# Performance work log

Hardware: AMD Instinct MI355X
Metric: run time of the kernel (lower is better)

## Reference

```python
import jax, jax.numpy as jnp
import numpy as np

N = 100000   # nodes
E = 1250000  # edges
F_IN = 64    # node feature dim
H = 64       # hidden_channels
B = 256      # graphs in batch
C = 2        # num_classes


def setup_inputs() -> dict:
    key = jax.random.key(0)
    ks = jax.random.split(key, 12)
    x = jax.random.normal(ks[0], (N, F_IN), dtype=jnp.float32)
    edge_index = jax.random.randint(ks[1], (2, E), 0, N, dtype=jnp.int64)
    batch = jnp.sort(jax.random.randint(ks[2], (N,), 0, B, dtype=jnp.int64))
    s = 1.0 / np.sqrt(H)
    W1 = jax.random.uniform(ks[3], (F_IN, H), jnp.float32, -s, s)
    b1 = jnp.zeros((H,), jnp.float32)
    W2 = jax.random.uniform(ks[4], (H, H), jnp.float32, -s, s)
    b2 = jnp.zeros((H,), jnp.float32)
    W3 = jax.random.uniform(ks[5], (H, H), jnp.float32, -s, s)
    b3 = jnp.zeros((H,), jnp.float32)
    Wl = jax.random.uniform(ks[6], (H, C), jnp.float32, -s, s)
    bl = jnp.zeros((C,), jnp.float32)
    return {"x": x, "edge_index": edge_index, "batch": batch,
            "W1": W1, "b1": b1, "W2": W2, "b2": b2, "W3": W3, "b3": b3,
            "Wl": Wl, "bl": bl}


def gcn_conv(x, W, b, src, dst, dinv_sqrt):
    # PyG GCNConv: h = x @ W; symmetric normalization with self-loops;
    # self-loop contribution handled analytically (norm = 1/deg).
    h = x @ W                                   # [N, H]
    norm = dinv_sqrt[src] * dinv_sqrt[dst]      # [E]
    msg = norm[:, None] * h[src]                # [E, H]
    agg = jax.ops.segment_sum(msg, dst, num_segments=x.shape[0])
    agg = agg + (dinv_sqrt * dinv_sqrt)[:, None] * h  # self loops
    return agg + b


def reference(x, edge_index, batch, W1, b1, W2, b2, W3, b3, Wl, bl):
    src, dst = edge_index[0], edge_index[1]
    # degree with self-loops (computed on target nodes, as in PyG)
    ones = jnp.ones((E,), jnp.float32)
    deg = jax.ops.segment_sum(ones, dst, num_segments=N) + 1.0
    dinv_sqrt = jax.lax.rsqrt(deg)

    h = jax.nn.relu(gcn_conv(x, W1, b1, src, dst, dinv_sqrt))
    h = jax.nn.relu(gcn_conv(h, W2, b2, src, dst, dinv_sqrt))
    h = gcn_conv(h, W3, b3, src, dst, dinv_sqrt)

    # global_mean_pool over batch vector
    sums = jax.ops.segment_sum(h, batch, num_segments=B)          # [B, H]
    cnts = jax.ops.segment_sum(jnp.ones((N,), jnp.float32), batch, num_segments=B)
    pooled = sums / jnp.maximum(cnts, 1.0)[:, None]

    # dropout(p=0.5) is identity in inference mode
    return pooled @ Wl + bl  # [B, C]
```

## Files before the change

kernel.cpp:

```cpp
#include <hip/hip_runtime.h>

#define NN 100000
#define EE 1250000
#define HH 64
#define BB 256
#define CC 2
#define NBLK 391
#define GBLK 2048
#define NWAVE (GBLK * 4)

__device__ __forceinline__ float lanebcast(float v, int k) {
    return __int_as_float(__builtin_amdgcn_readlane(__float_as_int(v), k));
}

__global__ void detect_i64(const int* __restrict__ raw, int* __restrict__ flag) {
    __shared__ int nonzero;
    if (threadIdx.x == 0) nonzero = 0;
    __syncthreads();
    int any = 0;
#pragma unroll
    for (int i = 0; i < 4; ++i) {
        int idx = 2 * (threadIdx.x + i * 256) + 1;
        if (raw[idx] != 0) any = 1;
    }
    if (any) atomicOr(&nonzero, 1);
    __syncthreads();
    if (threadIdx.x == 0) *flag = nonzero ? 0 : 1;
}

__global__ void count_kernel(const int* __restrict__ raw, const int* __restrict__ flag,
                             int* __restrict__ degi) {
    int e = blockIdx.x * 256 + threadIdx.x;
    if (e >= EE) return;
    int d = (*flag) ? raw[2 * (EE + e)] : raw[EE + e];
    atomicAdd(&degi[d], 1);
}

__global__ __launch_bounds__(256) void scan1(const int* __restrict__ degi,
                                             int* __restrict__ row,
                                             int* __restrict__ bsum,
                                             float* __restrict__ dinv) {
    __shared__ int s[256];
    int tid = threadIdx.x;
    int n = blockIdx.x * 256 + tid;
    int v = (n < NN) ? degi[n] : 0;
    int x = v;
    s[tid] = x;
    __syncthreads();
    for (int off = 1; off < 256; off <<= 1) {
        int t = (tid >= off) ? s[tid - off] : 0;
        __syncthreads();
        x += t;
        s[tid] = x;
        __syncthreads();
    }
    if (n < NN) {
        row[n] = x - v;
        dinv[n] = rsqrtf((float)v + 1.0f);
    }
    if (tid == 255) bsum[blockIdx.x] = x;
}

__global__ __launch_bounds__(512) void scan2(int* __restrict__ bsum) {
    __shared__ int s[512];
    int tid = threadIdx.x;
    int v = (tid < NBLK) ? bsum[tid] : 0;
    int x = v;
    s[tid] = x;
    __syncthreads();
    for (int off = 1; off < 512; off <<= 1) {
        int t = (tid >= off) ? s[tid - off] : 0;
        __syncthreads();
        x += t;
        s[tid] = x;
        __syncthreads();
    }
    if (tid < NBLK) bsum[tid] = x - v;
}

__global__ void scan3(int* __restrict__ row, const int* __restrict__ bsum) {
    int n = blockIdx.x * 256 + threadIdx.x;
    if (n < NN) row[n] += bsum[blockIdx.x];
    if (n == 0) row[NN] = EE;
}

__global__ void fill_kernel(const int* __restrict__ raw, const int* __restrict__ flag,
                            const float* __restrict__ dinv,
                            const int* __restrict__ row, int* __restrict__ fill,
                            int2* __restrict__ esort) {
    int e = blockIdx.x * 256 + threadIdx.x;
    if (e >= EE) return;
    int flg = *flag;
    int s = flg ? raw[2 * e]        : raw[e];
    int d = flg ? raw[2 * (EE + e)] : raw[EE + e];
    int pos = row[d] + atomicAdd(&fill[d], 1);
    float nm = dinv[s] * dinv[d];
    esort[pos] = make_int2(s, __float_as_int(nm));
}

__global__ __launch_bounds__(256) void gemm_reg(const float* __restrict__ X,
                                                const float* __restrict__ W,
                                                float* __restrict__ Hout) {
    int lane = threadIdx.x & 63;
    int gw = (blockIdx.x * 256 + threadIdx.x) >> 6;
    float Wreg[64];
#pragma unroll
    for (int k = 0; k < 64; ++k) Wreg[k] = W[k * 64 + lane];
    for (int n = gw; n < NN; n += NWAVE) {
        float xv = X[(size_t)n * 64 + lane];
        float a0 = 0.f, a1 = 0.f;
#pragma unroll
        for (int k = 0; k < 64; k += 2) {
            a0 = fmaf(lanebcast(xv, k),     Wreg[k],     a0);
            a1 = fmaf(lanebcast(xv, k + 1), Wreg[k + 1], a1);
        }
        Hout[(size_t)n * 64 + lane] = a0 + a1;
    }
}

template <int FUSE>
__global__ __launch_bounds__(256) void gather_kernel(
        const int* __restrict__ row, const int2* __restrict__ esort,
        const float* __restrict__ H, const float* __restrict__ dinv,
        const float* __restrict__ bias, const float* __restrict__ Wn,
        float* __restrict__ Out) {
    int lane = threadIdx.x & 63;
    int gw = (blockIdx.x * 256 + threadIdx.x) >> 6;

    float Wreg[FUSE ? 64 : 1];
    if constexpr (FUSE) {
#pragma unroll
        for (int k = 0; k < 64; ++k) Wreg[k] = Wn[k * 64 + lane];
    }
    float bv = bias[lane];

    for (int n = gw; n < NN; n += NWAVE) {
        int beg = row[n], end = row[n + 1];
        float acc = 0.0f;
        for (int base = beg; base < end; base += 64) {
            int cnt = end - base; if (cnt > 64) cnt = 64;
            int2 meta = (lane < cnt) ? esort[base + lane] : make_int2(0, 0);
            int cntp = (cnt + 7) & ~7;
            for (int j = 0; j < cntp; j += 8) {
                float hv[8], wv[8];
#pragma unroll
                for (int i = 0; i < 8; ++i) {
                    int s = __shfl(meta.x, j + i, 64);
                    wv[i] = __int_as_float(__shfl(meta.y, j + i, 64));
                    hv[i] = H[(size_t)s * 64 + lane];
                }
#pragma unroll
                for (int i = 0; i < 8; ++i) acc = fmaf(wv[i], hv[i], acc);
            }
        }
        float di = dinv[n];
        float agg = acc + di * di * H[(size_t)n * 64 + lane] + bv;
        if constexpr (FUSE) {
            float av = fmaxf(agg, 0.0f);
            float a0 = 0.f, a1 = 0.f;
#pragma unroll
            for (int k = 0; k < 64; k += 2) {
                a0 = fmaf(lanebcast(av, k),     Wreg[k],     a0);
                a1 = fmaf(lanebcast(av, k + 1), Wreg[k + 1], a1);
            }
            Out[(size_t)n * 64 + lane] = a0 + a1;
        } else {
            Out[(size_t)n * 64 + lane] = agg;
        }
    }
}

__global__ __launch_bounds__(256) void pool_kernel(
        const float* __restrict__ H, const int* __restrict__ braw,
        const int* __restrict__ flag,
        float* __restrict__ pooled, float* __restrict__ cnt) {
    int tid = threadIdx.x;
    int f = tid & 63, sub = tid >> 6;
    int flg = *flag;
    int base = blockIdx.x * 256 + sub * 64;
    float acc = 0.0f;
    int cur = -1, count = 0;
    for (int i = 0; i < 64; ++i) {
        int n = base + i;
        if (n >= NN) break;
        int g = flg ? braw[2 * n] : braw[n];
        if (g != cur) {
            if (cur >= 0) {
                atomicAdd(&pooled[cur * 64 + f], acc);
                if (f == 0) atomicAdd(&cnt[cur], (float)count);
            }
            cur = g; acc = 0.0f; count = 0;
        }
        acc += H[(size_t)n * 64 + f];
        ++count;
    }
    if (cur >= 0) {
        atomicAdd(&pooled[cur * 64 + f], acc);
        if (f == 0) atomicAdd(&cnt[cur], (float)count);
    }
}

__global__ __launch_bounds__(512) void final_linear(
        const float* __restrict__ pooled, const float* __restrict__ cnt,
        const float* __restrict__ Wl, const float* __restrict__ bl,
        float* __restrict__ out) {
    int t = threadIdx.x;
    int b = t >> 1, c = t & 1;
    float inv = 1.0f / fmaxf(cnt[b], 1.0f);
    float acc = 0.0f;
#pragma unroll
    for (int fi = 0; fi < 64; ++fi)
        acc += pooled[b * 64 + fi] * Wl[fi * 2 + c];
    out[t] = acc * inv + bl[c];
}

static inline size_t align256(size_t x) { return (x + 255) & ~size_t(255); }

extern "C" void kernel_launch(void* const* d_in, const int* in_sizes, int n_in,
                              void* d_out, int out_size, void* d_ws, size_t ws_size,
                              hipStream_t stream) {
    const float* x   = (const float*)d_in[0];
    const int*  eraw = (const int*)d_in[1];
    const int*  braw = (const int*)d_in[2];
    const float* W1 = (const float*)d_in[3];
    const float* b1 = (const float*)d_in[4];
    const float* W2 = (const float*)d_in[5];
    const float* b2 = (const float*)d_in[6];
    const float* W3 = (const float*)d_in[7];
    const float* b3 = (const float*)d_in[8];
    const float* Wl = (const float*)d_in[9];
    const float* bl = (const float*)d_in[10];
    float* out = (float*)d_out;

    char* ws = (char*)d_ws;
    size_t off = 0;
    int*   flag   = (int*)(ws + off);   off = align256(off + 256);
    size_t zoff = off;
    int*   degi   = (int*)(ws + off);   off = align256(off + (size_t)NN * 4);
    int*   fillc  = (int*)(ws + off);   off = align256(off + (size_t)NN * 4);
    float* pooled = (float*)(ws + off); off = align256(off + (size_t)BB * HH * 4);
    float* cnt    = (float*)(ws + off); off = align256(off + (size_t)BB * 4);
    size_t zlen = off - zoff;
    float* dinv   = (float*)(ws + off); off = align256(off + (size_t)NN * 4);
    int*   row    = (int*)(ws + off);   off = align256(off + (size_t)(NN + 1) * 4);
    int*   bsum   = (int*)(ws + off);   off = align256(off + (size_t)NBLK * 4);
    int2*  esort  = (int2*)(ws + off);  off = align256(off + (size_t)EE * 8);
    float* hA     = (float*)(ws + off); off = align256(off + (size_t)NN * HH * 4);
    float* hB     = (float*)(ws + off); off = align256(off + (size_t)NN * HH * 4);
    float* hC     = (float*)(ws + off); off = align256(off + (size_t)NN * HH * 4);

    const int eBlocks = (EE + 255) / 256;

    detect_i64<<<1, 256, 0, stream>>>(eraw, flag);
    hipMemsetAsync(ws + zoff, 0, zlen, stream);

    count_kernel<<<eBlocks, 256, 0, stream>>>(eraw, flag, degi);
    scan1<<<NBLK, 256, 0, stream>>>(degi, row, bsum, dinv);
    scan2<<<1, 512, 0, stream>>>(bsum);
    scan3<<<NBLK, 256, 0, stream>>>(row, bsum);
    fill_kernel<<<eBlocks, 256, 0, stream>>>(eraw, flag, dinv, row, fillc, esort);

    gemm_reg<<<GBLK, 256, 0, stream>>>(x, W1, hA);
    gather_kernel<1><<<GBLK, 256, 0, stream>>>(row, esort, hA, dinv, b1, W2, hB);
    gather_kernel<1><<<GBLK, 256, 0, stream>>>(row, esort, hB, dinv, b2, W3, hA);
    gather_kernel<0><<<GBLK, 256, 0, stream>>>(row, esort, hA, dinv, b3, nullptr, hC);

    pool_kernel<<<NBLK, 256, 0, stream>>>(hC, braw, flag, pooled, cnt);
    final_linear<<<1, 512, 0, stream>>>(pooled, cnt, Wl, bl, out);
}
```

Baseline: 381.1 us.

## Chunk features into 8-wide column slabs and pre-scale by dinv to shrink edge metadata

Stores node features in eight column-chunk slabs of 8 floats, each chunk processed by separate blocks, so each chunk's gather working set (about 3.2 MB) can stay cache-resident. Folds the symmetric normalization into the GEMM output (pre-multiplying by dinv of the source node), so edge metadata shrinks to a 4-byte source index with no per-edge weight. It unfuses the next-layer GEMM from the gather into separate launches and uses nontemporal loads and stores. The cost is extra kernel launches, a full feature-matrix round trip per layer, and the row offsets and edge indices being re-read by all eight chunks.

```diff
diff --git a/kernel.cpp b/kernel.cpp
--- a/kernel.cpp
+++ b/kernel.cpp
@@ -6,8 +6,12 @@
 #define BB 256
 #define CC 2
 #define NBLK 391
-#define GBLK 2048
-#define NWAVE (GBLK * 4)
+#define CS ((size_t)NN * 8)
+#define GEMM_BLK 2048
+#define GEMM_WAVES (GEMM_BLK * 4)
+#define GATH_BLK 16384
+#define WPC ((GATH_BLK / 8) * 4)
+#define NPAIR (NN / 2)
 
 __device__ __forceinline__ float lanebcast(float v, int k) {
     return __int_as_float(__builtin_amdgcn_readlane(__float_as_int(v), k));
@@ -85,97 +89,112 @@
 }
 
 __global__ void fill_kernel(const int* __restrict__ raw, const int* __restrict__ flag,
-                            const float* __restrict__ dinv,
                             const int* __restrict__ row, int* __restrict__ fill,
-                            int2* __restrict__ esort) {
+                            int* __restrict__ esrc) {
     int e = blockIdx.x * 256 + threadIdx.x;
     if (e >= EE) return;
     int flg = *flag;
     int s = flg ? raw[2 * e]        : raw[e];
     int d = flg ? raw[2 * (EE + e)] : raw[EE + e];
     int pos = row[d] + atomicAdd(&fill[d], 1);
-    float nm = dinv[s] * dinv[d];
-    esort[pos] = make_int2(s, __float_as_int(nm));
-}
-
-__global__ __launch_bounds__(256) void gemm_reg(const float* __restrict__ X,
-                                                const float* __restrict__ W,
-                                                float* __restrict__ Hout) {
+    esrc[pos] = s;
+}
+
+template <int IN_ROW>
+__global__ __launch_bounds__(256) void gemm_scaled(
+        const float* __restrict__ X, const float* __restrict__ W,
+        const float* __restrict__ dinv, float* __restrict__ Gout) {
     int lane = threadIdx.x & 63;
     int gw = (blockIdx.x * 256 + threadIdx.x) >> 6;
     float Wreg[64];
 #pragma unroll
     for (int k = 0; k < 64; ++k) Wreg[k] = W[k * 64 + lane];
-    for (int n = gw; n < NN; n += NWAVE) {
-        float xv = X[(size_t)n * 64 + lane];
+    int c = lane >> 3, fl = lane & 7;
+    for (int n = gw; n < NN; n += GEMM_WAVES) {
+        int nu = __builtin_amdgcn_readfirstlane(n);
+        float xv;
+        if constexpr (IN_ROW)
+            xv = __builtin_nontemporal_load(X + (size_t)nu * 64 + lane);
+        else
+            xv = __builtin_nontemporal_load(X + (size_t)c * CS + (size_t)nu * 8 + fl);
         float a0 = 0.f, a1 = 0.f;
 #pragma unroll
         for (int k = 0; k < 64; k += 2) {
             a0 = fmaf(lanebcast(xv, k),     Wreg[k],     a0);
             a1 = fmaf(lanebcast(xv, k + 1), Wreg[k + 1], a1);
         }
-        Hout[(size_t)n * 64 + lane] = a0 + a1;
-    }
-}
-
-template <int FUSE>
-__global__ __launch_bounds__(256) void gather_kernel(
-        const int* __restrict__ row, const int2* __restrict__ esort,
-        const float* __restrict__ H, const float* __restrict__ dinv,
-        const float* __restrict__ bias, const float* __restrict__ Wn,
-        float* __restrict__ Out) {
+        float r = (a0 + a1) * dinv[nu];
+        __builtin_nontemporal_store(r, Gout + (size_t)c * CS + (size_t)nu * 8 + fl);
+    }
+}
+
+template <int RELU>
+__global__ __launch_bounds__(256) void gather_chunk(
+        const int* __restrict__ row, const int* __restrict__ esrc,
+        const float* __restrict__ G, const float* __restrict__ dinv,
+        const float* __restrict__ bias, float* __restrict__ Out) {
     int lane = threadIdx.x & 63;
-    int gw = (blockIdx.x * 256 + threadIdx.x) >> 6;
-
-    float Wreg[FUSE ? 64 : 1];
-    if constexpr (FUSE) {
-#pragma unroll
-        for (int k = 0; k < 64; ++k) Wreg[k] = Wn[k * 64 + lane];
-    }
-    float bv = bias[lane];
-
-    for (int n = gw; n < NN; n += NWAVE) {
-        int beg = row[n], end = row[n + 1];
-        float acc = 0.0f;
-        for (int base = beg; base < end; base += 64) {
-            int cnt = end - base; if (cnt > 64) cnt = 64;
-            int2 meta = (lane < cnt) ? esort[base + lane] : make_int2(0, 0);
-            int cntp = (cnt + 7) & ~7;
-            for (int j = 0; j < cntp; j += 8) {
-                float hv[8], wv[8];
-#pragma unroll
-                for (int i = 0; i < 8; ++i) {
-                    int s = __shfl(meta.x, j + i, 64);
-                    wv[i] = __int_as_float(__shfl(meta.y, j + i, 64));
-                    hv[i] = H[(size_t)s * 64 + lane];
-                }
-#pragma unroll
-                for (int i = 0; i < 8; ++i) acc = fmaf(wv[i], hv[i], acc);
-            }
-        }
-        float di = dinv[n];
-        float agg = acc + di * di * H[(size_t)n * 64 + lane] + bv;
-        if constexpr (FUSE) {
-            float av = fmaxf(agg, 0.0f);
-            float a0 = 0.f, a1 = 0.f;
-#pragma unroll
-            for (int k = 0; k < 64; k += 2) {
-                a0 = fmaf(lanebcast(av, k),     Wreg[k],     a0);
-                a1 = fmaf(lanebcast(av, k + 1), Wreg[k + 1], a1);
-            }
-            Out[(size_t)n * 64 + lane] = a0 + a1;
-        } else {
-            Out[(size_t)n * 64 + lane] = agg;
+    int chunk = blockIdx.x & 7;
+    int wv = ((blockIdx.x >> 3) << 2) + (threadIdx.x >> 6);
+    int fl = lane & 7, eg = lane >> 3;
+    const float* __restrict__ Gc = G + (size_t)chunk * CS;
+    float bv = bias[chunk * 8 + fl];
+
+    for (int p = wv; p < NPAIR; p += WPC) {
+        int nu = __builtin_amdgcn_readfirstlane(p) * 2;
+        int b0 = row[nu], m = row[nu + 1], e1 = row[nu + 2];
+
+        float acc0 = 0.f;
+        for (int base = b0; base < m; base += 16) {
+            int v0 = base + eg, v1 = v0 + 8;
+            int c0 = v0 < m ? v0 : m - 1;
+            int c1 = v1 < m ? v1 : m - 1;
+            int s0 = __builtin_nontemporal_load(esrc + c0);
+            int s1 = __builtin_nontemporal_load(esrc + c1);
+            float g0 = Gc[(size_t)s0 * 8 + fl];
+            float g1 = Gc[(size_t)s1 * 8 + fl];
+            acc0 += (v0 < m ? g0 : 0.f) + (v1 < m ? g1 : 0.f);
+        }
+        float acc1 = 0.f;
+        for (int base = m; base < e1; base += 16) {
+            int v0 = base + eg, v1 = v0 + 8;
+            int c0 = v0 < e1 ? v0 : e1 - 1;
+            int c1 = v1 < e1 ? v1 : e1 - 1;
+            int s0 = __builtin_nontemporal_load(esrc + c0);
+            int s1 = __builtin_nontemporal_load(esrc + c1);
+            float g0 = Gc[(size_t)s0 * 8 + fl];
+            float g1 = Gc[(size_t)s1 * 8 + fl];
+            acc1 += (v0 < e1 ? g0 : 0.f) + (v1 < e1 ? g1 : 0.f);
+        }
+
+        acc0 += __shfl_xor(acc0, 8, 64);
+        acc0 += __shfl_xor(acc0, 16, 64);
+        acc0 += __shfl_xor(acc0, 32, 64);
+        acc1 += __shfl_xor(acc1, 8, 64);
+        acc1 += __shfl_xor(acc1, 16, 64);
+        acc1 += __shfl_xor(acc1, 32, 64);
+
+        float d0 = dinv[nu], d1 = dinv[nu + 1];
+        float gs0 = Gc[(size_t)nu * 8 + fl];
+        float gs1 = Gc[(size_t)(nu + 1) * 8 + fl];
+        float o0 = fmaf(acc0 + gs0, d0, bv);
+        float o1 = fmaf(acc1 + gs1, d1, bv);
+        if constexpr (RELU) { o0 = fmaxf(o0, 0.f); o1 = fmaxf(o1, 0.f); }
+        if (lane < 16) {
+            float ov = (lane < 8) ? o0 : o1;
+            __builtin_nontemporal_store(
+                ov, Out + (size_t)chunk * CS + (size_t)(nu + (lane >> 3)) * 8 + fl);
         }
     }
 }
 
 __global__ __launch_bounds__(256) void pool_kernel(
-        const float* __restrict__ H, const int* __restrict__ braw,
+        const float* __restrict__ Hc, const int* __restrict__ braw,
         const int* __restrict__ flag,
         float* __restrict__ pooled, float* __restrict__ cnt) {
     int tid = threadIdx.x;
     int f = tid & 63, sub = tid >> 6;
+    int c = f >> 3, fl = f & 7;
     int flg = *flag;
     int base = blockIdx.x * 256 + sub * 64;
     float acc = 0.0f;
@@ -191,7 +210,7 @@
             }
             cur = g; acc = 0.0f; count = 0;
         }
-        acc += H[(size_t)n * 64 + f];
+        acc += Hc[(size_t)c * CS + (size_t)n * 8 + fl];
         ++count;
     }
     if (cur >= 0) {
@@ -244,10 +263,9 @@
     float* dinv   = (float*)(ws + off); off = align256(off + (size_t)NN * 4);
     int*   row    = (int*)(ws + off);   off = align256(off + (size_t)(NN + 1) * 4);
     int*   bsum   = (int*)(ws + off);   off = align256(off + (size_t)NBLK * 4);
-    int2*  esort  = (int2*)(ws + off);  off = align256(off + (size_t)EE * 8);
-    float* hA     = (float*)(ws + off); off = align256(off + (size_t)NN * HH * 4);
-    float* hB     = (float*)(ws + off); off = align256(off + (size_t)NN * HH * 4);
-    float* hC     = (float*)(ws + off); off = align256(off + (size_t)NN * HH * 4);
+    int*   esrc   = (int*)(ws + off);   off = align256(off + (size_t)EE * 4);
+    float* bufA   = (float*)(ws + off); off = align256(off + (size_t)NN * HH * 4);
+    float* bufB   = (float*)(ws + off); off = align256(off + (size_t)NN * HH * 4);
 
     const int eBlocks = (EE + 255) / 256;
 
@@ -258,13 +276,15 @@
     scan1<<<NBLK, 256, 0, stream>>>(degi, row, bsum, dinv);
     scan2<<<1, 512, 0, stream>>>(bsum);
     scan3<<<NBLK, 256, 0, stream>>>(row, bsum);
-    fill_kernel<<<eBlocks, 256, 0, stream>>>(eraw, flag, dinv, row, fillc, esort);
-
-    gemm_reg<<<GBLK, 256, 0, stream>>>(x, W1, hA);
-    gather_kernel<1><<<GBLK, 256, 0, stream>>>(row, esort, hA, dinv, b1, W2, hB);
-    gather_kernel<1><<<GBLK, 256, 0, stream>>>(row, esort, hB, dinv, b2, W3, hA);
-    gather_kernel<0><<<GBLK, 256, 0, stream>>>(row, esort, hA, dinv, b3, nullptr, hC);
-
-    pool_kernel<<<NBLK, 256, 0, stream>>>(hC, braw, flag, pooled, cnt);
+    fill_kernel<<<eBlocks, 256, 0, stream>>>(eraw, flag, row, fillc, esrc);
+
+    gemm_scaled<1><<<GEMM_BLK, 256, 0, stream>>>(x, W1, dinv, bufA);
+    gather_chunk<1><<<GATH_BLK, 256, 0, stream>>>(row, esrc, bufA, dinv, b1, bufB);
+    gemm_scaled<0><<<GEMM_BLK, 256, 0, stream>>>(bufB, W2, dinv, bufA);
+    gather_chunk<1><<<GATH_BLK, 256, 0, stream>>>(row, esrc, bufA, dinv, b2, bufB);
+    gemm_scaled<0><<<GEMM_BLK, 256, 0, stream>>>(bufB, W3, dinv, bufA);
+    gather_chunk<0><<<GATH_BLK, 256, 0, stream>>>(row, esrc, bufA, dinv, b3, bufB);
+
+    pool_kernel<<<NBLK, 256, 0, stream>>>(bufB, braw, flag, pooled, cnt);
     final_linear<<<1, 512, 0, stream>>>(pooled, cnt, Wl, bl, out);
 }
```

Result: slower. 707.1 us (+85.5%).
